# Optimization experiments

Hardware: AMD Instinct MI355X
Metric: run time of the kernel (lower is better)

The kernel has to match this reference:

```python
import jax, jax.numpy as jnp
import numpy as np

B, DIN, H, NACT = 8192, 1025, 1024, 1026
NHEAD = 513  # npatches + STOP
K = 32       # kR = kS


def _make_seq(key, batch, n, k):
    k_idx, k_len = jax.random.split(key)
    # distinct indices per row: top-k of a random permutation
    perm = jnp.argsort(jax.random.uniform(k_idx, (batch, n)), axis=1)[:, :k]
    seq_len = jax.random.randint(k_len, (batch,), 1, k + 1).astype(jnp.int32)
    mask = jnp.arange(k)[None, :] < seq_len[:, None]
    seq_idx = jnp.where(mask, perm, -1).astype(jnp.int32)
    return seq_idx, seq_len


def setup_inputs() -> dict:
    key = jax.random.key(0)
    ks = jax.random.split(key, 8)
    state = jax.random.normal(ks[0], (B, DIN), dtype=jnp.float32)
    W0 = jax.random.normal(ks[1], (DIN, H), dtype=jnp.float32) * (2.0 / DIN) ** 0.5
    b0 = jnp.zeros((H,), jnp.float32)
    W1 = jax.random.normal(ks[2], (H, H), dtype=jnp.float32) * (2.0 / H) ** 0.5
    b1 = jnp.zeros((H,), jnp.float32)
    W2 = jax.random.normal(ks[3], (H, NACT), dtype=jnp.float32) * 0.01
    b2 = jnp.zeros((NACT,), jnp.float32)
    seq_idx_R, seq_len_R = _make_seq(ks[4], B, NHEAD, K)
    seq_idx_S, seq_len_S = _make_seq(ks[5], B, NHEAD, K)
    return {"state": state, "W0": W0, "b0": b0, "W1": W1, "b1": b1,
            "W2": W2, "b2": b2,
            "seq_idx_R": seq_idx_R, "seq_len_R": seq_len_R,
            "seq_idx_S": seq_idx_S, "seq_len_S": seq_len_S}


def _mlp(state, W0, b0, W1, b1, W2, b2):
    h = jax.nn.relu(state @ W0 + b0)
    h = jax.nn.relu(h @ W1 + b1)
    return h @ W2 + b2  # (B, NACT) logits


def _logprob_entropy_wo_replacement(logits, seq_idx, seq_len):
    # Faithful vectorized version of logprob_entropy_wo_replacement_batched.
    bsz, n = logits.shape
    col = jnp.arange(n)[None, :]
    neg_inf = jnp.float32(-jnp.inf)

    def step(carry, xs):
        remaining, logp, ent = carry          # (B,N) bool, (B,), (B,)
        t, idx_t = xs                          # scalar, (B,)
        active = t < seq_len                   # (B,)
        masked_logits = jnp.where(remaining, logits, neg_inf)
        lp = jax.nn.log_softmax(masked_logits, axis=-1)
        p = jnp.exp(lp)
        mp = jnp.where(remaining, p, 0.0)
        mlp_ = jnp.where(remaining, lp, 0.0)
        ent_step = -jnp.sum(mp * mlp_, axis=-1)
        ent = ent + jnp.where(active, ent_step, 0.0)
        valid = active & (idx_t >= 0)
        idx_safe = jnp.where(valid, idx_t, 0)
        g = jnp.take_along_axis(lp, idx_safe[:, None], axis=1)[:, 0]
        logp = logp + jnp.where(valid, g, 0.0)
        hit = (col == idx_safe[:, None]) & valid[:, None]
        remaining = remaining & ~hit
        return (remaining, logp, ent), None

    init = (jnp.ones((bsz, n), bool), jnp.zeros((bsz,), jnp.float32),
            jnp.zeros((bsz,), jnp.float32))
    ts = jnp.arange(seq_idx.shape[1], dtype=jnp.int32)
    (_, logp, ent), _ = jax.lax.scan(step, init, (ts, seq_idx.T))
    return logp, ent


def reference(state, W0, b0, W1, b1, W2, b2,
              seq_idx_R, seq_len_R, seq_idx_S, seq_len_S):
    x = _mlp(state, W0, b0, W1, b1, W2, b2)
    logpR, entR = _logprob_entropy_wo_replacement(x[:, :NHEAD], seq_idx_R, seq_len_R)
    logpS, entS = _logprob_entropy_wo_replacement(x[:, NHEAD:NHEAD + NHEAD], seq_idx_S, seq_len_S)
    # rows: [total logprob, total entropy] as in get_log_prob's (logpR+logpS, entR+entS)
    return jnp.stack([logpR + logpS, entR + entS], axis=0)  # (2, B)
```

## Files before the change

kernel.cpp:

```cpp
#include <hip/hip_runtime.h>
#include <cstdint>
#include <cstddef>

#define BATCH 8192
#define DIN   1025
#define HID   1024
#define NACT  1026
#define NHEAD 513
#define KSEL  32
#define KP0   1088
#define NP2   1152

typedef unsigned short u16;
typedef short bf16x8 __attribute__((ext_vector_type(8)));
typedef float f32x4 __attribute__((ext_vector_type(4)));

__device__ __forceinline__ u16 f2bf(float f) {
  unsigned u = __float_as_uint(f);
  u += 0x7fff + ((u >> 16) & 1);
  return (u16)(u >> 16);
}
__device__ __forceinline__ float bf2f(u16 h) {
  return __uint_as_float((unsigned)h << 16);
}

__device__ __forceinline__ void async_cp16(const u16* g, u16* l) {
  __builtin_amdgcn_global_load_lds((const __attribute__((address_space(1))) void*)g,
                                   (__attribute__((address_space(3))) void*)l,
                                   16, 0, 0);
}


__global__ void cvt_state(const float* __restrict__ in, u16* __restrict__ out) {
  int idx = blockIdx.x * 256 + threadIdx.x;
  const int QPR = KP0 / 4;
  if (idx >= BATCH * QPR) return;
  int r  = idx / QPR;
  int c4 = (idx - r * QPR) * 4;
  const float* src = in + (size_t)r * DIN + c4;
  ushort4 o;
  if (c4 + 3 < DIN) {
    o.x = f2bf(src[0]); o.y = f2bf(src[1]); o.z = f2bf(src[2]); o.w = f2bf(src[3]);
  } else {
    o.x = (c4 + 0 < DIN) ? f2bf(src[0]) : 0;
    o.y = (c4 + 1 < DIN) ? f2bf(src[1]) : 0;
    o.z = (c4 + 2 < DIN) ? f2bf(src[2]) : 0;
    o.w = (c4 + 3 < DIN) ? f2bf(src[3]) : 0;
  }
  *(ushort4*)(out + (size_t)r * KP0 + c4) = o;
}

__global__ void cvt_w_all(const float* __restrict__ W0, const float* __restrict__ W1,
                          const float* __restrict__ W2,
                          u16* __restrict__ W0t, u16* __restrict__ W1t,
                          u16* __restrict__ W2t) {
  const float* W; u16* Wt; int K, N, Kp, Np;
  if (blockIdx.z == 0)      { W = W0; Wt = W0t; K = DIN; N = HID;  Kp = KP0; Np = HID; }
  else if (blockIdx.z == 1) { W = W1; Wt = W1t; K = HID; N = HID;  Kp = HID; Np = HID; }
  else                      { W = W2; Wt = W2t; K = HID; N = NACT; Kp = HID; Np = NP2; }
  int k0 = blockIdx.y * 32, n0 = blockIdx.x * 32;
  if (k0 >= Kp || n0 >= Np) return;
  __shared__ float tile[32][33];
  int tx = threadIdx.x, ty = threadIdx.y;
#pragma unroll
  for (int i = 0; i < 32; i += 8) {
    int k = k0 + ty + i, n = n0 + tx;
    tile[ty + i][tx] = (k < K && n < N) ? W[(size_t)k * N + n] : 0.f;
  }
  __syncthreads();
#pragma unroll
  for (int i = 0; i < 32; i += 8) {
    int n = n0 + ty + i, k = k0 + tx;
    if (n < Np && k < Kp) Wt[(size_t)n * Kp + k] = f2bf(tile[tx][ty + i]);
  }
}


template<bool RELU, bool OBF16, int NT>
__global__ __launch_bounds__(256, 4)
void gemm_bt(const u16* __restrict__ A, const u16* __restrict__ Bt,
             const float* __restrict__ bias, int nbias,
             void* __restrict__ Cout, int ldc, int K)
{
  __shared__ __align__(16) u16 lds[12288];
  u16* ldsA = lds;
  u16* ldsB = lds + 4096;

  const int d     = blockIdx.x;
  const int group = d / (8 * NT);
  const int rsub  = d - group * (8 * NT);
  const int ntile = rsub >> 3;
  const int mtile = group * 8 + (rsub & 7);

  const int tid   = threadIdx.x;
  const int wave  = tid >> 6;
  const int lane  = tid & 63;
  const int waveM = wave >> 1, waveN = wave & 1;
  const int lr = lane & 15, lq = lane >> 4;
  const size_t bm = (size_t)mtile * 64;
  const size_t bn = (size_t)ntile * 128;

  const int cw  = wave * 64 + lane;
  const int row = cw >> 3;
  const int g   = (cw & 7) ^ (row & 7);
  const u16* gA0 = A  + (bm + row) * K + g * 8;
  const u16* gB0 = Bt + (bn + row) * K + g * 8;
  u16* lA0 = ldsA + wave * 512;
  u16* lB0 = ldsB + wave * 512;

  f32x4 acc[2][4] = {};

  const int r7 = lr & 7;
  const int s0 = lq ^ r7;
  const int s1 = (lq + 4) ^ r7;
  const u16* pa = ldsA + (waveM * 32 + lr) * 64;
  const u16* pb = ldsB + (waveN * 64 + lr) * 64;

  for (int k0 = 0; k0 < K; k0 += 64) {
#pragma unroll
    for (int j = 0; j < 2; ++j)
      async_cp16(gA0 + j * 32 * (size_t)K + k0, lA0 + j * 2048);
#pragma unroll
    for (int j = 0; j < 4; ++j)
      async_cp16(gB0 + j * 32 * (size_t)K + k0, lB0 + j * 2048);
    __syncthreads();

#pragma unroll
    for (int kk = 0; kk < 2; ++kk) {
      const int s = kk ? s1 : s0;
      bf16x8 af[2], bf[4];
#pragma unroll
      for (int t = 0; t < 2; ++t) af[t] = *(const bf16x8*)(pa + t * 1024 + s * 8);
#pragma unroll
      for (int t = 0; t < 4; ++t) bf[t] = *(const bf16x8*)(pb + t * 1024 + s * 8);
#pragma unroll
      for (int tm = 0; tm < 2; ++tm)
#pragma unroll
        for (int tn = 0; tn < 4; ++tn)
          acc[tm][tn] = __builtin_amdgcn_mfma_f32_16x16x32_bf16(af[tm], bf[tn], acc[tm][tn], 0, 0, 0);
    }
    __syncthreads();
  }

#pragma unroll
  for (int tm = 0; tm < 2; ++tm) {
    size_t rw = bm + waveM * 32 + tm * 16 + lq * 4;
#pragma unroll
    for (int tn = 0; tn < 4; ++tn) {
      int col = (int)bn + waveN * 64 + tn * 16 + lr;
      float bv = (col < nbias) ? bias[col] : 0.f;
#pragma unroll
      for (int r = 0; r < 4; ++r) {
        float v = acc[tm][tn][r] + bv;
        if (RELU) v = fmaxf(v, 0.f);
        if (OBF16) ((u16*)Cout)[(rw + r) * ldc + col] = f2bf(v);
        else       ((float*)Cout)[(rw + r) * ldc + col] = v;
      }
    }
  }
}


__global__ void sample_k(const u16* __restrict__ logits,
                         const int* __restrict__ idxR, const int* __restrict__ lenR,
                         const int* __restrict__ idxS, const int* __restrict__ lenS,
                         float* __restrict__ out)
{
  const int row  = blockIdx.x;
  const int w    = threadIdx.x >> 6;
  const int lane = threadIdx.x & 63;
  const u16* x = logits + (size_t)row * NP2 + w * NHEAD;
  const int* sidx = (w ? idxS : idxR) + (size_t)row * KSEL;
  const int slen  = (w ? lenS : lenR)[row];

  float m = -3.4e38f;
  for (int i = lane; i < NHEAD; i += 64) m = fmaxf(m, bf2f(x[i]));
#pragma unroll
  for (int d = 32; d; d >>= 1) m = fmaxf(m, __shfl_xor(m, d, 64));

  float S = 0.f, T = 0.f;
  for (int i = lane; i < NHEAD; i += 64) {
    float xi = bf2f(x[i]);
    float e = __expf(xi - m);
    S += e; T += e * xi;
  }
#pragma unroll
  for (int d = 32; d; d >>= 1) { S += __shfl_xor(S, d, 64); T += __shfl_xor(T, d, 64); }

  float e = 0.f, ex = 0.f, xt = 0.f;
  int active = (lane < KSEL) && (lane < slen);
  int valid = 0;
  if (active) {
    int id = sidx[lane];
    if (id >= 0) {
      valid = 1;
      xt = bf2f(x[id]);
      e  = __expf(xt - m);
      ex = e * xt;
    }
  }
  float pe = e, pex = ex;
#pragma unroll
  for (int d = 1; d < 32; d <<= 1) {
    float a = __shfl_up(pe, d, 64);
    float b = __shfl_up(pex, d, 64);
    if (lane >= d) { pe += a; pex += b; }
  }
  float lp = 0.f, en = 0.f;
  if (active) {
    float St = S - (pe - e);
    float Tt = T - (pex - ex);
    float logZ = m + __logf(St);
    en = logZ - Tt / St;
    if (valid) lp = xt - logZ;
  }
#pragma unroll
  for (int d = 32; d; d >>= 1) { lp += __shfl_xor(lp, d, 64); en += __shfl_xor(en, d, 64); }

  __shared__ float sh[4];
  if (lane == 0) { sh[w * 2] = lp; sh[w * 2 + 1] = en; }
  __syncthreads();
  if (threadIdx.x == 0) {
    out[row]         = sh[0] + sh[2];
    out[BATCH + row] = sh[1] + sh[3];
  }
}


extern "C" void kernel_launch(void* const* d_in, const int* in_sizes, int n_in,
                              void* d_out, int out_size, void* d_ws, size_t ws_size,
                              hipStream_t stream) {
  (void)in_sizes; (void)n_in; (void)out_size; (void)ws_size;
  const float* state = (const float*)d_in[0];
  const float* W0 = (const float*)d_in[1];
  const float* b0 = (const float*)d_in[2];
  const float* W1 = (const float*)d_in[3];
  const float* b1 = (const float*)d_in[4];
  const float* W2 = (const float*)d_in[5];
  const float* b2 = (const float*)d_in[6];
  const int* idxR = (const int*)d_in[7];
  const int* lenR = (const int*)d_in[8];
  const int* idxS = (const int*)d_in[9];
  const int* lenS = (const int*)d_in[10];
  float* out = (float*)d_out;

  char* ws = (char*)d_ws;
  size_t off = 0;
  auto alloc = [&](size_t bytes) -> char* {
    char* p = ws + off;
    off = (off + bytes + 255) & ~(size_t)255;
    return p;
  };
  u16* As     = (u16*)alloc((size_t)BATCH * KP0 * 2);
  u16* W0t    = (u16*)alloc((size_t)HID * KP0 * 2);
  u16* W1t    = (u16*)alloc((size_t)HID * HID * 2);
  u16* W2t    = (u16*)alloc((size_t)NP2 * HID * 2);
  u16* h1     = (u16*)alloc((size_t)BATCH * HID * 2);
  u16* lgts   = (u16*)alloc((size_t)BATCH * NP2 * 2);
  u16* h2 = As;

  cvt_state<<<(BATCH * (KP0 / 4) + 255) / 256, 256, 0, stream>>>(state, As);
  cvt_w_all<<<dim3(NP2 / 32, KP0 / 32, 3), dim3(32, 8), 0, stream>>>(W0, W1, W2, W0t, W1t, W2t);

  gemm_bt<true,  true, 8><<<(BATCH / 64) * (HID / 128), 256, 0, stream>>>(As, W0t, b0, HID,  h1,   HID, KP0);
  gemm_bt<true,  true, 8><<<(BATCH / 64) * (HID / 128), 256, 0, stream>>>(h1, W1t, b1, HID,  h2,   HID, HID);
  gemm_bt<false, true, 9><<<(BATCH / 64) * (NP2 / 128), 256, 0, stream>>>(h2, W2t, b2, NACT, lgts, NP2, HID);

  sample_k<<<BATCH, 128, 0, stream>>>(lgts, idxR, lenR, idxS, lenS, out);
}
```

Baseline: 206.1 us.

## Replace LDS-staged GEMM with direct global-to-register MFMA GEMM on larger tiles

Drops the LDS staging in the MLP GEMMs, where tiles were copied with global_load_lds and synchronized with barriers. Each wave now loads its A and B fragments straight from global memory into registers and issues MFMAs on a 64x64 per-wave tile. The block tile grows to 128x128, K becomes a compile-time constant with a fully unrolled loop, and occupancy hint drops to 2. This removes barrier and LDS traffic, but operands are no longer shared across waves, so it relies on L1/L2 for reuse and uses many more registers.

```diff
diff --git a/kernel.cpp b/kernel.cpp
--- a/kernel.cpp
+++ b/kernel.cpp
@@ -22,12 +22,6 @@
 }
 __device__ __forceinline__ float bf2f(u16 h) {
   return __uint_as_float((unsigned)h << 16);
-}
-
-__device__ __forceinline__ void async_cp16(const u16* g, u16* l) {
-  __builtin_amdgcn_global_load_lds((const __attribute__((address_space(1))) void*)g,
-                                   (__attribute__((address_space(3))) void*)l,
-                                   16, 0, 0);
 }
 
 
@@ -76,16 +70,12 @@
 }
 
 
-template<bool RELU, bool OBF16, int NT>
-__global__ __launch_bounds__(256, 4)
-void gemm_bt(const u16* __restrict__ A, const u16* __restrict__ Bt,
-             const float* __restrict__ bias, int nbias,
-             void* __restrict__ Cout, int ldc, int K)
+template<bool RELU, bool OBF16, int NT, int K>
+__global__ __launch_bounds__(256, 2)
+void gemm_direct(const u16* __restrict__ A, const u16* __restrict__ Bt,
+                 const float* __restrict__ bias, int nbias,
+                 void* __restrict__ Cout, int ldc)
 {
-  __shared__ __align__(16) u16 lds[12288];
-  u16* ldsA = lds;
-  u16* ldsB = lds + 4096;
-
   const int d     = blockIdx.x;
   const int group = d / (8 * NT);
   const int rsub  = d - group * (8 * NT);
@@ -95,59 +85,39 @@
   const int tid   = threadIdx.x;
   const int wave  = tid >> 6;
   const int lane  = tid & 63;
-  const int waveM = wave >> 1, waveN = wave & 1;
   const int lr = lane & 15, lq = lane >> 4;
-  const size_t bm = (size_t)mtile * 64;
-  const size_t bn = (size_t)ntile * 128;
-
-  const int cw  = wave * 64 + lane;
-  const int row = cw >> 3;
-  const int g   = (cw & 7) ^ (row & 7);
-  const u16* gA0 = A  + (bm + row) * K + g * 8;
-  const u16* gB0 = Bt + (bn + row) * K + g * 8;
-  u16* lA0 = ldsA + wave * 512;
-  u16* lB0 = ldsB + wave * 512;
-
-  f32x4 acc[2][4] = {};
-
-  const int r7 = lr & 7;
-  const int s0 = lq ^ r7;
-  const int s1 = (lq + 4) ^ r7;
-  const u16* pa = ldsA + (waveM * 32 + lr) * 64;
-  const u16* pb = ldsB + (waveN * 64 + lr) * 64;
-
-  for (int k0 = 0; k0 < K; k0 += 64) {
-#pragma unroll
-    for (int j = 0; j < 2; ++j)
-      async_cp16(gA0 + j * 32 * (size_t)K + k0, lA0 + j * 2048);
-#pragma unroll
-    for (int j = 0; j < 4; ++j)
-      async_cp16(gB0 + j * 32 * (size_t)K + k0, lB0 + j * 2048);
-    __syncthreads();
-
-#pragma unroll
-    for (int kk = 0; kk < 2; ++kk) {
-      const int s = kk ? s1 : s0;
-      bf16x8 af[2], bf[4];
-#pragma unroll
-      for (int t = 0; t < 2; ++t) af[t] = *(const bf16x8*)(pa + t * 1024 + s * 8);
-#pragma unroll
-      for (int t = 0; t < 4; ++t) bf[t] = *(const bf16x8*)(pb + t * 1024 + s * 8);
-#pragma unroll
-      for (int tm = 0; tm < 2; ++tm)
-#pragma unroll
-        for (int tn = 0; tn < 4; ++tn)
-          acc[tm][tn] = __builtin_amdgcn_mfma_f32_16x16x32_bf16(af[tm], bf[tn], acc[tm][tn], 0, 0, 0);
-    }
-    __syncthreads();
-  }
-
-#pragma unroll
-  for (int tm = 0; tm < 2; ++tm) {
-    size_t rw = bm + waveM * 32 + tm * 16 + lq * 4;
+  const size_t bm = (size_t)mtile * 128 + (wave >> 1) * 64;
+  const size_t bn = (size_t)ntile * 128 + (wave & 1) * 64;
+
+  const u16* pa[4]; const u16* pb[4];
+#pragma unroll
+  for (int t = 0; t < 4; ++t) {
+    pa[t] = A  + (bm + t * 16 + lr) * (size_t)K + lq * 8;
+    pb[t] = Bt + (bn + t * 16 + lr) * (size_t)K + lq * 8;
+  }
+
+  f32x4 acc[4][4] = {};
+
+#pragma unroll
+  for (int k0 = 0; k0 < K; k0 += 32) {
+    bf16x8 af[4], bf[4];
+#pragma unroll
+    for (int t = 0; t < 4; ++t) af[t] = *(const bf16x8*)(pa[t] + k0);
+#pragma unroll
+    for (int t = 0; t < 4; ++t) bf[t] = *(const bf16x8*)(pb[t] + k0);
+#pragma unroll
+    for (int tm = 0; tm < 4; ++tm)
+#pragma unroll
+      for (int tn = 0; tn < 4; ++tn)
+        acc[tm][tn] = __builtin_amdgcn_mfma_f32_16x16x32_bf16(af[tm], bf[tn], acc[tm][tn], 0, 0, 0);
+  }
+
+#pragma unroll
+  for (int tm = 0; tm < 4; ++tm) {
+    size_t rw = bm + tm * 16 + lq * 4;
 #pragma unroll
     for (int tn = 0; tn < 4; ++tn) {
-      int col = (int)bn + waveN * 64 + tn * 16 + lr;
+      int col = (int)bn + tn * 16 + lr;
       float bv = (col < nbias) ? bias[col] : 0.f;
 #pragma unroll
       for (int r = 0; r < 4; ++r) {
@@ -262,9 +232,9 @@
   cvt_state<<<(BATCH * (KP0 / 4) + 255) / 256, 256, 0, stream>>>(state, As);
   cvt_w_all<<<dim3(NP2 / 32, KP0 / 32, 3), dim3(32, 8), 0, stream>>>(W0, W1, W2, W0t, W1t, W2t);
 
-  gemm_bt<true,  true, 8><<<(BATCH / 64) * (HID / 128), 256, 0, stream>>>(As, W0t, b0, HID,  h1,   HID, KP0);
-  gemm_bt<true,  true, 8><<<(BATCH / 64) * (HID / 128), 256, 0, stream>>>(h1, W1t, b1, HID,  h2,   HID, HID);
-  gemm_bt<false, true, 9><<<(BATCH / 64) * (NP2 / 128), 256, 0, stream>>>(h2, W2t, b2, NACT, lgts, NP2, HID);
+  gemm_direct<true,  true, 8, KP0><<<(BATCH / 128) * (HID / 128) , 256, 0, stream>>>(As, W0t, b0, HID,  h1,   HID);
+  gemm_direct<true,  true, 8, HID><<<(BATCH / 128) * (HID / 128) , 256, 0, stream>>>(h1, W1t, b1, HID,  h2,   HID);
+  gemm_direct<false, true, 9, HID><<<(BATCH / 128) * (NP2 / 128) , 256, 0, stream>>>(h2, W2t, b2, NACT, lgts, NP2);
 
   sample_k<<<BATCH, 128, 0, stream>>>(lgts, idxR, lenR, idxS, lenS, out);
 }
```

New measurement: 344.3 us. 1.67x slower.
